# Kernel tuning notes

Measured on AMD Instinct MI355X. Metric: run time of the kernel, lower is better.

Reference implementation:

```python
import jax, jax.numpy as jnp
import numpy as np

B, S, H, I, E, K = 1, 2048, 1024, 512, 16, 4


def setup_inputs() -> dict:
    key = jax.random.key(0)
    k0, k1, k2, k3, k4, k5 = jax.random.split(key, 6)
    hidden_states = jax.random.normal(k0, (B, S, H), jnp.float32)
    T = B * S
    topk_idx = jax.random.randint(k1, (T, K), 0, E, dtype=jnp.int32)
    raw = jax.random.uniform(k2, (T, K), jnp.float32)
    topk_weight = raw / jnp.sum(raw, axis=-1, keepdims=True)  # normalized top-k gate weights
    scale = 0.02
    w_gate = jax.random.normal(k3, (E, H, I), jnp.float32) * scale
    w_up = jax.random.normal(k4, (E, H, I), jnp.float32) * scale
    w_down = jax.random.normal(k5, (E, I, H), jnp.float32) * scale
    return {
        "hidden_states": hidden_states,
        "topk_idx": topk_idx,
        "topk_weight": topk_weight,
        "w_gate": w_gate,
        "w_up": w_up,
        "w_down": w_down,
    }


def reference(hidden_states, topk_idx, topk_weight, w_gate, w_up, w_down):
    # hidden_states: [B,S,H]; topk_idx/topk_weight: [T,K]; w_*: [E,H,I]/[E,I,H]
    b, s, h = hidden_states.shape
    t = b * s
    e = w_gate.shape[0]
    x = hidden_states.reshape(t, h)
    # routing_weights.scatter_(1, topk_idx, topk_weight)
    routing_weights = jnp.zeros((t, e), x.dtype).at[
        jnp.arange(t)[:, None], topk_idx
    ].set(topk_weight)
    # per-expert gated MLP over all tokens (math identical to masked dispatch:
    # tokens with routing weight 0 contribute nothing)
    g = jnp.einsum("th,ehi->eti", x, w_gate)  # [E,T,I]
    u = jnp.einsum("th,ehi->eti", x, w_up)
    d = jnp.einsum("eti,eih->eth", jax.nn.silu(g) * u, w_down)  # [E,T,H]
    out = jnp.einsum("eth,te->th", d, routing_weights)  # weighted combine
    return out.reshape(b, s, h)
```

## Files before the change

### kernel.cpp

```cpp
#include <hip/hip_runtime.h>
#include <hip/hip_bf16.h>
#include <stdint.h>

#define HH 1024
#define II 512
#define EE 16
#define TT 2048
#define KTOP 4
#define PP (TT * KTOP)
#define MAXROWS 12288

typedef unsigned short u16;
typedef unsigned int u32;
typedef __attribute__((ext_vector_type(8))) short short8;
typedef __attribute__((ext_vector_type(4))) float f32x4;
typedef __attribute__((ext_vector_type(4))) unsigned short u16x4;
typedef __attribute__((ext_vector_type(8))) unsigned short u16x8;

__device__ __forceinline__ u16 f2bf(float f) {
  union { float f; unsigned u; } v; v.f = f;
  unsigned r = v.u + 0x7fffu + ((v.u >> 16) & 1u);
  return (u16)(r >> 16);
}
__device__ __forceinline__ float bf2f(u16 b) {
  union { unsigned u; float f; } v; v.u = ((unsigned)b) << 16; return v.f;
}
__device__ __forceinline__ short f2bf_hw(float f) {
  __hip_bfloat16 h = __float2bfloat16(f);
  union { __hip_bfloat16 h; short s; } v; v.h = h; return v.s;
}

__device__ __forceinline__ void gld16(const u16* g, u16* l) {
  __builtin_amdgcn_global_load_lds(
      (const __attribute__((address_space(1))) unsigned int*)g,
      (__attribute__((address_space(3))) unsigned int*)l, 16, 0, 0);
}

__global__ __launch_bounds__(1024) void prep_small(
    const float* __restrict__ x, const int* __restrict__ tidx,
    const float* __restrict__ tw,
    u16* __restrict__ xb,
    int* __restrict__ perm, float* __restrict__ wt, int* __restrict__ rowof,
    int* __restrict__ tile_e, int* __restrict__ tile_r,
    int* __restrict__ ntiles) {
  __shared__ int s_e[PP];
  __shared__ int whist[16][16];
  __shared__ int wbase[16][16];
  __shared__ int pad_lo[EE], pad_hi[EE];

  const int bid = blockIdx.x;
  const int tid = threadIdx.x;

  if (bid == 0) {
    const int lane = tid & 63;
    const int wv = tid >> 6;

#pragma unroll
    for (int i = 0; i < 2; i++) {
      const int t = tid + i * 1024;
      const int4 v = ((const int4*)tidx)[t];
      const bool v0 = (v.x != v.y) && (v.x != v.z) && (v.x != v.w);
      const bool v1 = (v.y != v.z) && (v.y != v.w);
      const bool v2 = (v.z != v.w);
      s_e[t * 4 + 0] = v.x | (v0 ? 16 : 0);
      s_e[t * 4 + 1] = v.y | (v1 ? 16 : 0);
      s_e[t * 4 + 2] = v.z | (v2 ? 16 : 0);
      s_e[t * 4 + 3] = v.w | 16;
    }
    __syncthreads();

    int h0, h1, h2, h3, h4, h5, h6, h7, h8, h9, h10, h11, h12, h13, h14, h15;
    h0=h1=h2=h3=h4=h5=h6=h7=h8=h9=h10=h11=h12=h13=h14=h15=0;
    const unsigned long long ltm = (1ull << lane) - 1ull;
    for (int c = 0; c < 8; c++) {
      const int p = (wv << 9) + (c << 6) + lane;
      const int se = s_e[p];
      const int e = se & 15;
      const bool valid = (se & 16) != 0;
      int rank = 0;
#define RANK_STEP(J, HJ)                                            \
      {                                                             \
        unsigned long long m = __ballot(valid && (e == J));         \
        if (valid && (e == J)) rank = HJ + __popcll(m & ltm);       \
        HJ += __popcll(m);                                          \
      }
      RANK_STEP(0, h0)  RANK_STEP(1, h1)  RANK_STEP(2, h2)  RANK_STEP(3, h3)
      RANK_STEP(4, h4)  RANK_STEP(5, h5)  RANK_STEP(6, h6)  RANK_STEP(7, h7)
      RANK_STEP(8, h8)  RANK_STEP(9, h9)  RANK_STEP(10, h10) RANK_STEP(11, h11)
      RANK_STEP(12, h12) RANK_STEP(13, h13) RANK_STEP(14, h14) RANK_STEP(15, h15)
#undef RANK_STEP
      if (valid) s_e[p] = se | (rank << 16);
    }
    if (lane == 0) {
      whist[wv][0] = h0;   whist[wv][1] = h1;   whist[wv][2] = h2;   whist[wv][3] = h3;
      whist[wv][4] = h4;   whist[wv][5] = h5;   whist[wv][6] = h6;   whist[wv][7] = h7;
      whist[wv][8] = h8;   whist[wv][9] = h9;   whist[wv][10] = h10; whist[wv][11] = h11;
      whist[wv][12] = h12; whist[wv][13] = h13; whist[wv][14] = h14; whist[wv][15] = h15;
    }
    __syncthreads();

    if (tid == 0) {
      int off = 0, nt = 0;
      for (int j = 0; j < EE; j++) {
        int tot = 0;
        for (int w = 0; w < 16; w++) { wbase[w][j] = off + tot; tot += whist[w][j]; }
        const int cap = (tot + 127) & ~127;
        pad_lo[j] = off + tot;
        pad_hi[j] = off + cap;
        for (int m0 = 0; m0 < cap; m0 += 128) { tile_e[nt] = j; tile_r[nt] = off + m0; nt++; }
        off += cap;
      }
      *ntiles = nt;
    }
    __syncthreads();

#pragma unroll
    for (int i = 0; i < 8; i++) {
      const int p = i * 1024 + tid;
      const int se = s_e[p];
      int pos = -1;
      if (se & 16) {
        const int e = se & 15;
        const int r = se >> 16;
        pos = wbase[p >> 9][e] + r;
        perm[pos] = p >> 2;
        wt[pos] = tw[p];
      }
      rowof[p] = pos;
    }
    for (int j = 0; j < EE; j++) {
      const int lo = pad_lo[j], hi = pad_hi[j];
      for (int i = lo + tid; i < hi; i += 1024) {
        perm[i] = 0;
        wt[i] = 0.f;
      }
    }
    return;
  }

  const int base = ((bid - 1) * 1024 + tid) * 16;
  f32x4 v0 = *(const f32x4*)(x + base);
  f32x4 v1 = *(const f32x4*)(x + base + 4);
  f32x4 v2 = *(const f32x4*)(x + base + 8);
  f32x4 v3 = *(const f32x4*)(x + base + 12);
  u16x8 o0 = { f2bf(v0[0]), f2bf(v0[1]), f2bf(v0[2]), f2bf(v0[3]),
               f2bf(v1[0]), f2bf(v1[1]), f2bf(v1[2]), f2bf(v1[3]) };
  u16x8 o1 = { f2bf(v2[0]), f2bf(v2[1]), f2bf(v2[2]), f2bf(v2[3]),
               f2bf(v3[0]), f2bf(v3[1]), f2bf(v3[2]), f2bf(v3[3]) };
  *(u16x8*)(xb + base) = o0;
  *(u16x8*)(xb + base + 8) = o1;
}

__global__ __launch_bounds__(256) void gemm1_kernel(
    const u16* __restrict__ xb, const float* __restrict__ wg,
    const float* __restrict__ wu,
    const int* __restrict__ perm, const float* __restrict__ wt,
    const int* __restrict__ tile_e, const int* __restrict__ tile_r,
    const int* __restrict__ ntiles, u16* __restrict__ ACT) {
  const int tileid = blockIdx.y;
  if (tileid >= *ntiles) return;
  const int e = tile_e[tileid];
  const int row0 = tile_r[tileid];
  const int n0 = blockIdx.x * 64;

  __shared__ __align__(16) u16 As[128 * 64];

  const int tid = threadIdx.x;
  const int lane = tid & 63;
  const int wid = tid >> 6;
  const int fr = lane & 15, fq = lane >> 4;

  const int lrow = lane >> 3;
  const int sc8 = ((lane & 7) ^ lrow) * 8;

  const u16* gA[4]; u16* lA[4];
#pragma unroll
  for (int j = 0; j < 4; j++) {
    const int trow = j * 32 + wid * 8 + lrow;
    gA[j] = xb + (size_t)perm[row0 + trow] * HH + sc8;
    lA[j] = As + (j * 4 + wid) * 512;
  }

  const int ncol = n0 + wid * 16 + fr;
  const float* gbase = wg + (size_t)e * HH * II + ncol;
  const float* ubase = wu + (size_t)e * HH * II + ncol;

  f32x4 accg[8], accu[8];
  const f32x4 vz = {0.f, 0.f, 0.f, 0.f};
#pragma unroll
  for (int m = 0; m < 8; m++) { accg[m] = vz; accu[m] = vz; }

  for (int k0 = 0; k0 < HH; k0 += 64) {
    float fg[2][8], fu[2][8];
#pragma unroll
    for (int ks = 0; ks < 2; ks++)
#pragma unroll
      for (int j = 0; j < 8; j++) {
        const size_t koff = (size_t)(k0 + ks * 32 + fq * 8 + j) * II;
        fg[ks][j] = gbase[koff];
        fu[ks][j] = ubase[koff];
      }
    __syncthreads();
#pragma unroll
    for (int j = 0; j < 4; j++) gld16(gA[j] + k0, lA[j]);
    __syncthreads();

    short8 bg[2], bu[2];
#pragma unroll
    for (int ks = 0; ks < 2; ks++)
#pragma unroll
      for (int j = 0; j < 8; j++) {
        bg[ks][j] = f2bf_hw(fg[ks][j]);
        bu[ks][j] = f2bf_hw(fu[ks][j]);
      }

#pragma unroll
    for (int ks = 0; ks < 2; ks++)
#pragma unroll
      for (int m = 0; m < 8; m++) {
        const int r = m * 16 + fr;
        const short8 a = *(const short8*)(&As[r * 64 + (((ks * 4 + fq) ^ (r & 7)) * 8)]);
        accg[m] = __builtin_amdgcn_mfma_f32_16x16x32_bf16(a, bg[ks], accg[m], 0, 0, 0);
        accu[m] = __builtin_amdgcn_mfma_f32_16x16x32_bf16(a, bu[ks], accu[m], 0, 0, 0);
      }
  }

#pragma unroll
  for (int m = 0; m < 8; m++) {
#pragma unroll
    for (int jj = 0; jj < 4; jj++) {
      const int rloc = m * 16 + fq * 4 + jj;
      const float w = wt[row0 + rloc];
      const float g = accg[m][jj];
      const float u = accu[m][jj];
      const float s = g / (1.f + __expf(-g));
      ACT[(size_t)(row0 + rloc) * II + ncol] = f2bf(s * u * w);
    }
  }
}

__global__ __launch_bounds__(256) void gemm2_kernel(
    const u16* __restrict__ ACT, const float* __restrict__ wd,
    const int* __restrict__ tile_e, const int* __restrict__ tile_r,
    const int* __restrict__ ntiles, u16* __restrict__ D) {
  const int tileid = blockIdx.y;
  if (tileid >= *ntiles) return;
  const int e = tile_e[tileid];
  const int row0 = tile_r[tileid];
  const int n0 = blockIdx.x * 128;

  __shared__ __align__(16) u16 As[128 * 64];

  const int tid = threadIdx.x;
  const int lane = tid & 63;
  const int wid = tid >> 6;
  const int fr = lane & 15, fq = lane >> 4;

  const int lrow = lane >> 3;
  const int sc8 = ((lane & 7) ^ lrow) * 8;

  const u16* gA[4]; u16* lA[4];
#pragma unroll
  for (int j = 0; j < 4; j++) {
    const int trow = j * 32 + wid * 8 + lrow;
    gA[j] = ACT + (size_t)(row0 + trow) * II + sc8;
    lA[j] = As + (j * 4 + wid) * 512;
  }

  const int nc0 = n0 + wid * 32 + fr;
  const float* dbase = wd + (size_t)e * II * HH + nc0;

  f32x4 acc[8][2];
  const f32x4 vz = {0.f, 0.f, 0.f, 0.f};
#pragma unroll
  for (int m = 0; m < 8; m++) { acc[m][0] = vz; acc[m][1] = vz; }

  for (int k0 = 0; k0 < II; k0 += 64) {
    float fb[2][2][8];
#pragma unroll
    for (int nf = 0; nf < 2; nf++)
#pragma unroll
      for (int ks = 0; ks < 2; ks++)
#pragma unroll
        for (int j = 0; j < 8; j++)
          fb[nf][ks][j] = dbase[(size_t)(k0 + ks * 32 + fq * 8 + j) * HH + nf * 16];
    __syncthreads();
#pragma unroll
    for (int j = 0; j < 4; j++) gld16(gA[j] + k0, lA[j]);
    __syncthreads();

    short8 b[2][2];
#pragma unroll
    for (int nf = 0; nf < 2; nf++)
#pragma unroll
      for (int ks = 0; ks < 2; ks++)
#pragma unroll
        for (int j = 0; j < 8; j++)
          b[nf][ks][j] = f2bf_hw(fb[nf][ks][j]);

#pragma unroll
    for (int ks = 0; ks < 2; ks++)
#pragma unroll
      for (int m = 0; m < 8; m++) {
        const int r = m * 16 + fr;
        const short8 a = *(const short8*)(&As[r * 64 + (((ks * 4 + fq) ^ (r & 7)) * 8)]);
        acc[m][0] = __builtin_amdgcn_mfma_f32_16x16x32_bf16(a, b[0][ks], acc[m][0], 0, 0, 0);
        acc[m][1] = __builtin_amdgcn_mfma_f32_16x16x32_bf16(a, b[1][ks], acc[m][1], 0, 0, 0);
      }
  }

#pragma unroll
  for (int m = 0; m < 8; m++) {
#pragma unroll
    for (int jj = 0; jj < 4; jj++) {
      const int rloc = m * 16 + fq * 4 + jj;
      u16* dp = D + (size_t)(row0 + rloc) * HH + nc0;
      dp[0]  = f2bf(acc[m][0][jj]);
      dp[16] = f2bf(acc[m][1][jj]);
    }
  }
}

__global__ __launch_bounds__(256) void combine_kernel(
    const u16* __restrict__ D, const int* __restrict__ rowof,
    float* __restrict__ out) {
  const int t = blockIdx.x;
  const int h = threadIdx.x * 4;
  const int4 r4 = ((const int4*)rowof)[t];
  float a0 = 0.f, a1 = 0.f, a2 = 0.f, a3 = 0.f;
#define ACCUM(R)                                                     \
  if ((R) >= 0) {                                                    \
    u16x4 d = *(const u16x4*)(D + (size_t)(R) * HH + h);             \
    a0 += bf2f(d[0]); a1 += bf2f(d[1]); a2 += bf2f(d[2]); a3 += bf2f(d[3]); \
  }
  ACCUM(r4.x) ACCUM(r4.y) ACCUM(r4.z) ACCUM(r4.w)
#undef ACCUM
  float4 o = { a0, a1, a2, a3 };
  *(float4*)(out + (size_t)t * HH + h) = o;
}

extern "C" void kernel_launch(void* const* d_in, const int* in_sizes, int n_in,
                              void* d_out, int out_size, void* d_ws, size_t ws_size,
                              hipStream_t stream) {
  const float* x = (const float*)d_in[0];
  const int* tidx = (const int*)d_in[1];
  const float* tw = (const float*)d_in[2];
  const float* wg = (const float*)d_in[3];
  const float* wu = (const float*)d_in[4];
  const float* wd = (const float*)d_in[5];
  float* out = (float*)d_out;

  char* ws = (char*)d_ws;
  int* ntiles = (int*)(ws + 0);
  int* tile_e = (int*)(ws + 1024);
  int* tile_r = (int*)(ws + 2048);
  int* perm = (int*)(ws + 4096);
  float* wt = (float*)(ws + 53248);
  int* rowof = (int*)(ws + 102400);
  u16* xb = (u16*)(ws + 262144);
  u16* D = (u16*)(ws + 4456448);
  u16* ACT = (u16*)(ws + 54788096);

  prep_small<<<129, 1024, 0, stream>>>(x, tidx, tw, xb, perm, wt, rowof,
                                       tile_e, tile_r, ntiles);
  gemm1_kernel<<<dim3(II / 64, 80), 256, 0, stream>>>(xb, wg, wu, perm, wt,
                                                      tile_e, tile_r, ntiles, ACT);
  gemm2_kernel<<<dim3(HH / 128, 80), 256, 0, stream>>>(ACT, wd,
                                                       tile_e, tile_r, ntiles, D);
  combine_kernel<<<TT, 256, 0, stream>>>(D, rowof, out);
}
```

Measured before the change: 89.61 us.

## Double-buffer LDS and weight registers in both expert GEMM kernels

Both grouped GEMM kernels now use two LDS tiles and two register sets for the fp32 weight fragments. The next K-slice's global loads and LDS staging are issued before the current slice's MFMA compute, so memory latency overlaps with math and one barrier per step is removed. This doubles LDS use per block and raises register pressure, which may lower occupancy. It also relies on gld16 asynchronous completion being covered by the remaining barrier.

```diff
diff --git a/kernel.cpp b/kernel.cpp
--- a/kernel.cpp
+++ b/kernel.cpp
@@ -151,6 +151,41 @@
   *(u16x8*)(xb + base + 8) = o1;
 }
 
+#define G1_LOADB(FG, FU, K0)                                           \
+  _Pragma("unroll")                                                    \
+  for (int ks = 0; ks < 2; ks++)                                       \
+    _Pragma("unroll")                                                  \
+    for (int j = 0; j < 8; j++) {                                      \
+      const size_t koff = (size_t)((K0) + ks * 32 + fq * 8 + j) * II;  \
+      FG[ks][j] = gbase[koff];                                         \
+      FU[ks][j] = ubase[koff];                                         \
+    }
+
+#define G1_STAGE(BUF, K0)                                              \
+  _Pragma("unroll")                                                    \
+  for (int j = 0; j < 4; j++) gld16(gA[j] + (K0), (BUF) + (j * 4 + wid) * 512);
+
+#define G1_COMPUTE(FG, FU, ASBUF)                                      \
+  {                                                                    \
+    short8 bg[2], bu[2];                                               \
+    _Pragma("unroll")                                                  \
+    for (int ks = 0; ks < 2; ks++)                                     \
+      _Pragma("unroll")                                                \
+      for (int j = 0; j < 8; j++) {                                    \
+        bg[ks][j] = f2bf_hw(FG[ks][j]);                                \
+        bu[ks][j] = f2bf_hw(FU[ks][j]);                                \
+      }                                                                \
+    _Pragma("unroll")                                                  \
+    for (int ks = 0; ks < 2; ks++)                                     \
+      _Pragma("unroll")                                                \
+      for (int m = 0; m < 8; m++) {                                    \
+        const int r = m * 16 + fr;                                     \
+        const short8 a = *(const short8*)(&(ASBUF)[r * 64 + (((ks * 4 + fq) ^ (r & 7)) * 8)]); \
+        accg[m] = __builtin_amdgcn_mfma_f32_16x16x32_bf16(a, bg[ks], accg[m], 0, 0, 0); \
+        accu[m] = __builtin_amdgcn_mfma_f32_16x16x32_bf16(a, bu[ks], accu[m], 0, 0, 0); \
+      }                                                                \
+  }
+
 __global__ __launch_bounds__(256) void gemm1_kernel(
     const u16* __restrict__ xb, const float* __restrict__ wg,
     const float* __restrict__ wu,
@@ -163,7 +198,7 @@
   const int row0 = tile_r[tileid];
   const int n0 = blockIdx.x * 64;
 
-  __shared__ __align__(16) u16 As[128 * 64];
+  __shared__ __align__(16) u16 As[2][128 * 64];
 
   const int tid = threadIdx.x;
   const int lane = tid & 63;
@@ -173,13 +208,14 @@
   const int lrow = lane >> 3;
   const int sc8 = ((lane & 7) ^ lrow) * 8;
 
-  const u16* gA[4]; u16* lA[4];
+  const u16* gA[4];
 #pragma unroll
   for (int j = 0; j < 4; j++) {
     const int trow = j * 32 + wid * 8 + lrow;
     gA[j] = xb + (size_t)perm[row0 + trow] * HH + sc8;
-    lA[j] = As + (j * 4 + wid) * 512;
-  }
+  }
+  u16* const As0 = &As[0][0];
+  u16* const As1 = &As[1][0];
 
   const int ncol = n0 + wid * 16 + fr;
   const float* gbase = wg + (size_t)e * HH * II + ncol;
@@ -190,39 +226,23 @@
 #pragma unroll
   for (int m = 0; m < 8; m++) { accg[m] = vz; accu[m] = vz; }
 
-  for (int k0 = 0; k0 < HH; k0 += 64) {
-    float fg[2][8], fu[2][8];
-#pragma unroll
-    for (int ks = 0; ks < 2; ks++)
-#pragma unroll
-      for (int j = 0; j < 8; j++) {
-        const size_t koff = (size_t)(k0 + ks * 32 + fq * 8 + j) * II;
-        fg[ks][j] = gbase[koff];
-        fu[ks][j] = ubase[koff];
-      }
-    __syncthreads();
-#pragma unroll
-    for (int j = 0; j < 4; j++) gld16(gA[j] + k0, lA[j]);
-    __syncthreads();
-
-    short8 bg[2], bu[2];
-#pragma unroll
-    for (int ks = 0; ks < 2; ks++)
-#pragma unroll
-      for (int j = 0; j < 8; j++) {
-        bg[ks][j] = f2bf_hw(fg[ks][j]);
-        bu[ks][j] = f2bf_hw(fu[ks][j]);
-      }
-
-#pragma unroll
-    for (int ks = 0; ks < 2; ks++)
-#pragma unroll
-      for (int m = 0; m < 8; m++) {
-        const int r = m * 16 + fr;
-        const short8 a = *(const short8*)(&As[r * 64 + (((ks * 4 + fq) ^ (r & 7)) * 8)]);
-        accg[m] = __builtin_amdgcn_mfma_f32_16x16x32_bf16(a, bg[ks], accg[m], 0, 0, 0);
-        accu[m] = __builtin_amdgcn_mfma_f32_16x16x32_bf16(a, bu[ks], accu[m], 0, 0, 0);
-      }
+  float fgA[2][8], fuA[2][8], fgB[2][8], fuB[2][8];
+
+  G1_LOADB(fgA, fuA, 0)
+  G1_STAGE(As0, 0)
+  __syncthreads();
+
+  for (int t = 0; t < 16; t += 2) {
+    G1_LOADB(fgB, fuB, (t + 1) * 64)
+    G1_STAGE(As1, (t + 1) * 64)
+    G1_COMPUTE(fgA, fuA, As0)
+    __syncthreads();
+    if (t < 14) {
+      G1_LOADB(fgA, fuA, (t + 2) * 64)
+      G1_STAGE(As0, (t + 2) * 64)
+    }
+    G1_COMPUTE(fgB, fuB, As1)
+    __syncthreads();
   }
 
 #pragma unroll
@@ -238,6 +258,40 @@
     }
   }
 }
+
+#define G2_LOADB(FB, K0)                                               \
+  _Pragma("unroll")                                                    \
+  for (int nf = 0; nf < 2; nf++)                                       \
+    _Pragma("unroll")                                                  \
+    for (int ks = 0; ks < 2; ks++)                                     \
+      _Pragma("unroll")                                                \
+      for (int j = 0; j < 8; j++)                                      \
+        FB[nf][ks][j] = dbase[(size_t)((K0) + ks * 32 + fq * 8 + j) * HH + nf * 16];
+
+#define G2_STAGE(BUF, K0)                                              \
+  _Pragma("unroll")                                                    \
+  for (int j = 0; j < 4; j++) gld16(gA[j] + (K0), (BUF) + (j * 4 + wid) * 512);
+
+#define G2_COMPUTE(FB, ASBUF)                                          \
+  {                                                                    \
+    short8 b[2][2];                                                    \
+    _Pragma("unroll")                                                  \
+    for (int nf = 0; nf < 2; nf++)                                     \
+      _Pragma("unroll")                                                \
+      for (int ks = 0; ks < 2; ks++)                                   \
+        _Pragma("unroll")                                              \
+        for (int j = 0; j < 8; j++)                                    \
+          b[nf][ks][j] = f2bf_hw(FB[nf][ks][j]);                       \
+    _Pragma("unroll")                                                  \
+    for (int ks = 0; ks < 2; ks++)                                     \
+      _Pragma("unroll")                                                \
+      for (int m = 0; m < 8; m++) {                                    \
+        const int r = m * 16 + fr;                                     \
+        const short8 a = *(const short8*)(&(ASBUF)[r * 64 + (((ks * 4 + fq) ^ (r & 7)) * 8)]); \
+        acc[m][0] = __builtin_amdgcn_mfma_f32_16x16x32_bf16(a, b[0][ks], acc[m][0], 0, 0, 0); \
+        acc[m][1] = __builtin_amdgcn_mfma_f32_16x16x32_bf16(a, b[1][ks], acc[m][1], 0, 0, 0); \
+      }                                                                \
+  }
 
 __global__ __launch_bounds__(256) void gemm2_kernel(
     const u16* __restrict__ ACT, const float* __restrict__ wd,
@@ -249,7 +303,7 @@
   const int row0 = tile_r[tileid];
   const int n0 = blockIdx.x * 128;
 
-  __shared__ __align__(16) u16 As[128 * 64];
+  __shared__ __align__(16) u16 As[2][128 * 64];
 
   const int tid = threadIdx.x;
   const int lane = tid & 63;
@@ -259,13 +313,14 @@
   const int lrow = lane >> 3;
   const int sc8 = ((lane & 7) ^ lrow) * 8;
 
-  const u16* gA[4]; u16* lA[4];
+  const u16* gA[4];
 #pragma unroll
   for (int j = 0; j < 4; j++) {
     const int trow = j * 32 + wid * 8 + lrow;
     gA[j] = ACT + (size_t)(row0 + trow) * II + sc8;
-    lA[j] = As + (j * 4 + wid) * 512;
-  }
+  }
+  u16* const As0 = &As[0][0];
+  u16* const As1 = &As[1][0];
 
   const int nc0 = n0 + wid * 32 + fr;
   const float* dbase = wd + (size_t)e * II * HH + nc0;
@@ -275,38 +330,23 @@
 #pragma unroll
   for (int m = 0; m < 8; m++) { acc[m][0] = vz; acc[m][1] = vz; }
 
-  for (int k0 = 0; k0 < II; k0 += 64) {
-    float fb[2][2][8];
-#pragma unroll
-    for (int nf = 0; nf < 2; nf++)
-#pragma unroll
-      for (int ks = 0; ks < 2; ks++)
-#pragma unroll
-        for (int j = 0; j < 8; j++)
-          fb[nf][ks][j] = dbase[(size_t)(k0 + ks * 32 + fq * 8 + j) * HH + nf * 16];
-    __syncthreads();
-#pragma unroll
-    for (int j = 0; j < 4; j++) gld16(gA[j] + k0, lA[j]);
-    __syncthreads();
-
-    short8 b[2][2];
-#pragma unroll
-    for (int nf = 0; nf < 2; nf++)
-#pragma unroll
-      for (int ks = 0; ks < 2; ks++)
-#pragma unroll
-        for (int j = 0; j < 8; j++)
-          b[nf][ks][j] = f2bf_hw(fb[nf][ks][j]);
-
-#pragma unroll
-    for (int ks = 0; ks < 2; ks++)
-#pragma unroll
-      for (int m = 0; m < 8; m++) {
-        const int r = m * 16 + fr;
-        const short8 a = *(const short8*)(&As[r * 64 + (((ks * 4 + fq) ^ (r & 7)) * 8)]);
-        acc[m][0] = __builtin_amdgcn_mfma_f32_16x16x32_bf16(a, b[0][ks], acc[m][0], 0, 0, 0);
-        acc[m][1] = __builtin_amdgcn_mfma_f32_16x16x32_bf16(a, b[1][ks], acc[m][1], 0, 0, 0);
-      }
+  float fbA[2][2][8], fbB[2][2][8];
+
+  G2_LOADB(fbA, 0)
+  G2_STAGE(As0, 0)
+  __syncthreads();
+
+  for (int t = 0; t < 8; t += 2) {
+    G2_LOADB(fbB, (t + 1) * 64)
+    G2_STAGE(As1, (t + 1) * 64)
+    G2_COMPUTE(fbA, As0)
+    __syncthreads();
+    if (t < 6) {
+      G2_LOADB(fbA, (t + 2) * 64)
+      G2_STAGE(As0, (t + 2) * 64)
+    }
+    G2_COMPUTE(fbB, As1)
+    __syncthreads();
   }
 
 #pragma unroll
```

Result: faster. 85.93 us (-4.1%).

## Double-buffer A/B tiles in LDS with vectorized B loads and 2x2 warp tiling

Applied to the files above, without the earlier changes.

Both expert GEMM kernels now stage the fp32 weight tile through LDS as packed bf16 pairs, using 16-byte vector global loads instead of scalar strided loads per lane. A and B tiles are double-buffered so the next K-slice is loaded while the current one feeds MFMAs, with one barrier per iteration instead of two. Warps are rearranged into a 2x2 grid so each wave reuses A and B fragments across more MFMAs. The cost is more LDS per block, which may lower occupancy, plus extra LDS write/read traffic for B.

```diff
diff --git a/kernel.cpp b/kernel.cpp
--- a/kernel.cpp
+++ b/kernel.cpp
@@ -25,9 +25,9 @@
 __device__ __forceinline__ float bf2f(u16 b) {
   union { unsigned u; float f; } v; v.u = ((unsigned)b) << 16; return v.f;
 }
-__device__ __forceinline__ short f2bf_hw(float f) {
+__device__ __forceinline__ u16 f2bf_hw(float f) {
   __hip_bfloat16 h = __float2bfloat16(f);
-  union { __hip_bfloat16 h; short s; } v; v.h = h; return v.s;
+  union { __hip_bfloat16 h; u16 s; } v; v.h = h; return v.s;
 }
 
 __device__ __forceinline__ void gld16(const u16* g, u16* l) {
@@ -163,80 +163,123 @@
   const int row0 = tile_r[tileid];
   const int n0 = blockIdx.x * 64;
 
-  __shared__ __align__(16) u16 As[128 * 64];
+  __shared__ __align__(16) u16 As[2][128 * 64];
+  __shared__ __align__(16) u32 Bs[2][2][64 * 32];
 
   const int tid = threadIdx.x;
   const int lane = tid & 63;
   const int wid = tid >> 6;
+  const int wm = wid >> 1, wn = wid & 1;
   const int fr = lane & 15, fq = lane >> 4;
 
   const int lrow = lane >> 3;
   const int sc8 = ((lane & 7) ^ lrow) * 8;
 
-  const u16* gA[4]; u16* lA[4];
-#pragma unroll
-  for (int j = 0; j < 4; j++) {
-    const int trow = j * 32 + wid * 8 + lrow;
-    gA[j] = xb + (size_t)perm[row0 + trow] * HH + sc8;
-    lA[j] = As + (j * 4 + wid) * 512;
-  }
-
-  const int ncol = n0 + wid * 16 + fr;
-  const float* gbase = wg + (size_t)e * HH * II + ncol;
-  const float* ubase = wu + (size_t)e * HH * II + ncol;
-
-  f32x4 accg[8], accu[8];
+  const u16* gA[4];
+#pragma unroll
+  for (int j = 0; j < 4; j++)
+    gA[j] = xb + (size_t)perm[row0 + j * 32 + wid * 8 + lrow] * HH + sc8;
+
+  const int n4 = fr * 4;
+  const int kpl = wid * 8 + fq;
+  const float* gBm[2];
+  gBm[0] = wg + (size_t)e * HH * II + n0 + n4;
+  gBm[1] = wu + (size_t)e * HH * II + n0 + n4;
+
+  f32x4 accg[4][2], accu[4][2];
   const f32x4 vz = {0.f, 0.f, 0.f, 0.f};
 #pragma unroll
-  for (int m = 0; m < 8; m++) { accg[m] = vz; accu[m] = vz; }
-
-  for (int k0 = 0; k0 < HH; k0 += 64) {
-    float fg[2][8], fu[2][8];
-#pragma unroll
-    for (int ks = 0; ks < 2; ks++)
-#pragma unroll
-      for (int j = 0; j < 8; j++) {
-        const size_t koff = (size_t)(k0 + ks * 32 + fq * 8 + j) * II;
-        fg[ks][j] = gbase[koff];
-        fu[ks][j] = ubase[koff];
-      }
+  for (int m = 0; m < 4; m++)
+#pragma unroll
+    for (int n = 0; n < 2; n++) { accg[m][n] = vz; accu[m][n] = vz; }
+
+  f32x4 bl[2][2], bh[2][2];
+
+#define G1_LOADB(K0)                                                      \
+  _Pragma("unroll")                                                       \
+  for (int mt = 0; mt < 2; mt++)                                          \
+    _Pragma("unroll")                                                     \
+    for (int r = 0; r < 2; r++) {                                         \
+      const float* p = gBm[mt] + (size_t)((K0) + 2 * (kpl + r * 4)) * II; \
+      bl[mt][r] = *(const f32x4*)p;                                       \
+      bh[mt][r] = *(const f32x4*)(p + II);                                \
+    }
+
+#define G1_WRITEB(BP)                                                     \
+  _Pragma("unroll")                                                       \
+  for (int mt = 0; mt < 2; mt++)                                          \
+    _Pragma("unroll")                                                     \
+    for (int r = 0; r < 2; r++)                                           \
+      _Pragma("unroll")                                                   \
+      for (int i = 0; i < 4; i++) {                                       \
+        const int n = n4 + i;                                             \
+        const u32 pk = (u32)f2bf_hw(bl[mt][r][i]) |                       \
+                       ((u32)f2bf_hw(bh[mt][r][i]) << 16);                \
+        (BP)[mt * 2048 + n * 32 +                                         \
+             (((wid * 2 + r) ^ ((n >> 1) & 7)) * 4 | fq)] = pk;           \
+      }
+
+#define G1_STAGEA(DST, K0)                                                \
+  _Pragma("unroll")                                                       \
+  for (int j = 0; j < 4; j++) gld16(gA[j] + (K0), (DST) + (j * 4 + wid) * 512);
+
+#define G1_COMPUTE(ASRC, BP)                                              \
+  _Pragma("unroll")                                                       \
+  for (int ks = 0; ks < 2; ks++) {                                        \
+    short8 af[4];                                                         \
+    _Pragma("unroll")                                                     \
+    for (int m = 0; m < 4; m++) {                                         \
+      const int rr = wm * 64 + m * 16 + fr;                               \
+      af[m] = *(const short8*)&(ASRC)[rr * 64 + (((ks * 4 + fq) ^ (rr & 7)) * 8)]; \
+    }                                                                     \
+    _Pragma("unroll")                                                     \
+    for (int nn = 0; nn < 2; nn++) {                                      \
+      const int n = wn * 32 + nn * 16 + fr;                               \
+      const int bo = n * 32 + (((ks * 4 + fq) ^ ((n >> 1) & 7)) * 4);     \
+      const short8 bg = *(const short8*)&(BP)[bo];                        \
+      const short8 bu = *(const short8*)&(BP)[2048 + bo];                 \
+      _Pragma("unroll")                                                   \
+      for (int m = 0; m < 4; m++) {                                       \
+        accg[m][nn] = __builtin_amdgcn_mfma_f32_16x16x32_bf16(af[m], bg, accg[m][nn], 0, 0, 0); \
+        accu[m][nn] = __builtin_amdgcn_mfma_f32_16x16x32_bf16(af[m], bu, accu[m][nn], 0, 0, 0); \
+      }                                                                   \
+    }                                                                     \
+  }
+
+  u16* Acur = &As[0][0]; u16* Anxt = &As[1][0];
+  u32* Bcur = &Bs[0][0][0]; u32* Bnxt = &Bs[1][0][0];
+
+  G1_LOADB(0)
+  G1_STAGEA(Acur, 0)
+  G1_WRITEB(Bcur)
+  __syncthreads();
+
+  for (int t = 0; t < 16; t++) {
+    if (t < 15) {
+      G1_LOADB((t + 1) * 64)
+      G1_STAGEA(Anxt, (t + 1) * 64)
+    }
+    G1_COMPUTE(Acur, Bcur)
+    if (t < 15) G1_WRITEB(Bnxt)
     __syncthreads();
-#pragma unroll
-    for (int j = 0; j < 4; j++) gld16(gA[j] + k0, lA[j]);
-    __syncthreads();
-
-    short8 bg[2], bu[2];
-#pragma unroll
-    for (int ks = 0; ks < 2; ks++)
-#pragma unroll
-      for (int j = 0; j < 8; j++) {
-        bg[ks][j] = f2bf_hw(fg[ks][j]);
-        bu[ks][j] = f2bf_hw(fu[ks][j]);
-      }
-
-#pragma unroll
-    for (int ks = 0; ks < 2; ks++)
-#pragma unroll
-      for (int m = 0; m < 8; m++) {
-        const int r = m * 16 + fr;
-        const short8 a = *(const short8*)(&As[r * 64 + (((ks * 4 + fq) ^ (r & 7)) * 8)]);
-        accg[m] = __builtin_amdgcn_mfma_f32_16x16x32_bf16(a, bg[ks], accg[m], 0, 0, 0);
-        accu[m] = __builtin_amdgcn_mfma_f32_16x16x32_bf16(a, bu[ks], accu[m], 0, 0, 0);
-      }
-  }
-
-#pragma unroll
-  for (int m = 0; m < 8; m++) {
+    u16* ta = Acur; Acur = Anxt; Anxt = ta;
+    u32* tb = Bcur; Bcur = Bnxt; Bnxt = tb;
+  }
+
+#pragma unroll
+  for (int m = 0; m < 4; m++)
 #pragma unroll
     for (int jj = 0; jj < 4; jj++) {
-      const int rloc = m * 16 + fq * 4 + jj;
+      const int rloc = wm * 64 + m * 16 + fq * 4 + jj;
       const float w = wt[row0 + rloc];
-      const float g = accg[m][jj];
-      const float u = accu[m][jj];
-      const float s = g / (1.f + __expf(-g));
-      ACT[(size_t)(row0 + rloc) * II + ncol] = f2bf(s * u * w);
-    }
-  }
+#pragma unroll
+      for (int nn = 0; nn < 2; nn++) {
+        const float g = accg[m][nn][jj];
+        const float u = accu[m][nn][jj];
+        const float s = g / (1.f + __expf(-g));
+        ACT[(size_t)(row0 + rloc) * II + n0 + wn * 32 + nn * 16 + fr] = f2bf(s * u * w);
+      }
+    }
 }
 
 __global__ __launch_bounds__(256) void gemm2_kernel(
@@ -249,76 +292,112 @@
   const int row0 = tile_r[tileid];
   const int n0 = blockIdx.x * 128;
 
-  __shared__ __align__(16) u16 As[128 * 64];
+  __shared__ __align__(16) u16 As[2][128 * 64];
+  __shared__ __align__(16) u32 Bs[2][128 * 32];
 
   const int tid = threadIdx.x;
   const int lane = tid & 63;
   const int wid = tid >> 6;
+  const int wm = wid >> 1, wn = wid & 1;
   const int fr = lane & 15, fq = lane >> 4;
 
   const int lrow = lane >> 3;
   const int sc8 = ((lane & 7) ^ lrow) * 8;
 
-  const u16* gA[4]; u16* lA[4];
-#pragma unroll
-  for (int j = 0; j < 4; j++) {
-    const int trow = j * 32 + wid * 8 + lrow;
-    gA[j] = ACT + (size_t)(row0 + trow) * II + sc8;
-    lA[j] = As + (j * 4 + wid) * 512;
-  }
-
-  const int nc0 = n0 + wid * 32 + fr;
-  const float* dbase = wd + (size_t)e * II * HH + nc0;
-
-  f32x4 acc[8][2];
+  const u16* gA[4];
+#pragma unroll
+  for (int j = 0; j < 4; j++)
+    gA[j] = ACT + (size_t)(row0 + j * 32 + wid * 8 + lrow) * II + sc8;
+
+  const int n4 = fr * 4;
+  const int kpl = wid * 8 + fq;
+  const float* gB = wd + (size_t)e * II * HH + n0 + n4;
+
+  f32x4 acc[4][4];
   const f32x4 vz = {0.f, 0.f, 0.f, 0.f};
 #pragma unroll
-  for (int m = 0; m < 8; m++) { acc[m][0] = vz; acc[m][1] = vz; }
-
-  for (int k0 = 0; k0 < II; k0 += 64) {
-    float fb[2][2][8];
-#pragma unroll
-    for (int nf = 0; nf < 2; nf++)
-#pragma unroll
-      for (int ks = 0; ks < 2; ks++)
-#pragma unroll
-        for (int j = 0; j < 8; j++)
-          fb[nf][ks][j] = dbase[(size_t)(k0 + ks * 32 + fq * 8 + j) * HH + nf * 16];
+  for (int m = 0; m < 4; m++)
+#pragma unroll
+    for (int n = 0; n < 4; n++) acc[m][n] = vz;
+
+  f32x4 bl[2][2], bh[2][2];
+
+#define G2_LOADB(K0)                                                      \
+  _Pragma("unroll")                                                       \
+  for (int h = 0; h < 2; h++)                                             \
+    _Pragma("unroll")                                                     \
+    for (int r = 0; r < 2; r++) {                                         \
+      const float* p = gB + (size_t)((K0) + 2 * (kpl + r * 4)) * HH + h * 64; \
+      bl[h][r] = *(const f32x4*)p;                                        \
+      bh[h][r] = *(const f32x4*)(p + HH);                                 \
+    }
+
+#define G2_WRITEB(BP)                                                     \
+  _Pragma("unroll")                                                       \
+  for (int h = 0; h < 2; h++)                                             \
+    _Pragma("unroll")                                                     \
+    for (int r = 0; r < 2; r++)                                           \
+      _Pragma("unroll")                                                   \
+      for (int i = 0; i < 4; i++) {                                       \
+        const int n = h * 64 + n4 + i;                                    \
+        const u32 pk = (u32)f2bf_hw(bl[h][r][i]) |                        \
+                       ((u32)f2bf_hw(bh[h][r][i]) << 16);                 \
+        (BP)[n * 32 + (((wid * 2 + r) ^ ((n >> 1) & 7)) * 4 | fq)] = pk;  \
+      }
+
+#define G2_STAGEA(DST, K0)                                                \
+  _Pragma("unroll")                                                       \
+  for (int j = 0; j < 4; j++) gld16(gA[j] + (K0), (DST) + (j * 4 + wid) * 512);
+
+#define G2_COMPUTE(ASRC, BP)                                              \
+  _Pragma("unroll")                                                       \
+  for (int ks = 0; ks < 2; ks++) {                                        \
+    short8 af[4];                                                         \
+    _Pragma("unroll")                                                     \
+    for (int m = 0; m < 4; m++) {                                         \
+      const int rr = wm * 64 + m * 16 + fr;                               \
+      af[m] = *(const short8*)&(ASRC)[rr * 64 + (((ks * 4 + fq) ^ (rr & 7)) * 8)]; \
+    }                                                                     \
+    _Pragma("unroll")                                                     \
+    for (int nn = 0; nn < 4; nn++) {                                      \
+      const int n = wn * 64 + nn * 16 + fr;                               \
+      const short8 bb = *(const short8*)&(BP)[n * 32 + (((ks * 4 + fq) ^ ((n >> 1) & 7)) * 4)]; \
+      _Pragma("unroll")                                                   \
+      for (int m = 0; m < 4; m++)                                         \
+        acc[m][nn] = __builtin_amdgcn_mfma_f32_16x16x32_bf16(af[m], bb, acc[m][nn], 0, 0, 0); \
+    }                                                                     \
+  }
+
+  u16* Acur = &As[0][0]; u16* Anxt = &As[1][0];
+  u32* Bcur = &Bs[0][0]; u32* Bnxt = &Bs[1][0];
+
+  G2_LOADB(0)
+  G2_STAGEA(Acur, 0)
+  G2_WRITEB(Bcur)
+  __syncthreads();
+
+  for (int t = 0; t < 8; t++) {
+    if (t < 7) {
+      G2_LOADB((t + 1) * 64)
+      G2_STAGEA(Anxt, (t + 1) * 64)
+    }
+    G2_COMPUTE(Acur, Bcur)
+    if (t < 7) G2_WRITEB(Bnxt)
     __syncthreads();
-#pragma unroll
-    for (int j = 0; j < 4; j++) gld16(gA[j] + k0, lA[j]);
-    __syncthreads();
-
-    short8 b[2][2];
-#pragma unroll
-    for (int nf = 0; nf < 2; nf++)
-#pragma unroll
-      for (int ks = 0; ks < 2; ks++)
-#pragma unroll
-        for (int j = 0; j < 8; j++)
-          b[nf][ks][j] = f2bf_hw(fb[nf][ks][j]);
-
-#pragma unroll
-    for (int ks = 0; ks < 2; ks++)
-#pragma unroll
-      for (int m = 0; m < 8; m++) {
-        const int r = m * 16 + fr;
-        const short8 a = *(const short8*)(&As[r * 64 + (((ks * 4 + fq) ^ (r & 7)) * 8)]);
-        acc[m][0] = __builtin_amdgcn_mfma_f32_16x16x32_bf16(a, b[0][ks], acc[m][0], 0, 0, 0);
-        acc[m][1] = __builtin_amdgcn_mfma_f32_16x16x32_bf16(a, b[1][ks], acc[m][1], 0, 0, 0);
-      }
-  }
-
-#pragma unroll
-  for (int m = 0; m < 8; m++) {
+    u16* ta = Acur; Acur = Anxt; Anxt = ta;
+    u32* tb = Bcur; Bcur = Bnxt; Bnxt = tb;
+  }
+
+#pragma unroll
+  for (int m = 0; m < 4; m++)
 #pragma unroll
     for (int jj = 0; jj < 4; jj++) {
-      const int rloc = m * 16 + fq * 4 + jj;
-      u16* dp = D + (size_t)(row0 + rloc) * HH + nc0;
-      dp[0]  = f2bf(acc[m][0][jj]);
-      dp[16] = f2bf(acc[m][1][jj]);
-    }
-  }
+      const int rloc = wm * 64 + m * 16 + fq * 4 + jj;
+      u16* dp = D + (size_t)(row0 + rloc) * HH + n0 + wn * 64 + fr;
+#pragma unroll
+      for (int nn = 0; nn < 4; nn++)
+        dp[nn * 16] = f2bf(acc[m][nn][jj]);
+    }
 }
 
 __global__ __launch_bounds__(256) void combine_kernel(
```

New measurement: 97.73 us. 9.1% more time.
